# Optimization experiments

Measured on AMD Instinct MI355X. Metric: run time of the kernel, lower is better.

## Reference

```python
import jax, jax.numpy as jnp
import numpy as np

NEG_INF = -100000000.0  # matches masked_fill value in torch source

def setup_inputs() -> dict:
    key = jax.random.key(0)
    ks = jax.random.split(key, 7)
    d_model, d = 1024, 128
    B, S = 4, 2048
    scale = 1.0 / np.sqrt(d_model)
    x = jax.random.normal(ks[0], (B, S, d_model), dtype=jnp.float32)
    Wq = jax.random.normal(ks[1], (d, d_model), dtype=jnp.float32) * scale
    bq = jax.random.normal(ks[2], (d,), dtype=jnp.float32) * 0.02
    Wk = jax.random.normal(ks[3], (d, d_model), dtype=jnp.float32) * scale
    bk = jax.random.normal(ks[4], (d,), dtype=jnp.float32) * 0.02
    Wv = jax.random.normal(ks[5], (d, d_model), dtype=jnp.float32) * scale
    bv = jax.random.normal(ks[6], (d,), dtype=jnp.float32) * 0.02
    return {"x": x, "Wq": Wq, "bq": bq, "Wk": Wk, "bk": bk, "Wv": Wv, "bv": bv}

def reference(x, Wq, bq, Wk, bk, Wv, bv):
    # Q,K,V: [B,S,d] via torch Linear (x @ W.T + b)
    Q = jnp.einsum('bsm,dm->bsd', x, Wq) + bq
    K = jnp.einsum('bsm,dm->bsd', x, Wk) + bk
    V = jnp.einsum('bsm,dm->bsd', x, Wv) + bv
    d = Wk.shape[0]
    scale = 1.0 / jnp.sqrt(jnp.asarray(d, dtype=Q.dtype))
    scores = jnp.einsum('bqd,bkd->bqk', Q, K) * scale  # [B,S,S]
    # Faithful to source: tril then value-based mask (tril==0 -> -1e8).
    tril = jnp.tril(scores)
    masked = jnp.where(tril == 0, NEG_INF, tril)
    attn = jax.nn.softmax(masked, axis=-1)
    context = jnp.einsum('bqk,bkd->bqd', attn, V)
    return context
```

## Files before the change

kernel.cpp:

```cpp
#include <hip/hip_runtime.h>

typedef __attribute__((ext_vector_type(8))) short bf16x8;
typedef __attribute__((ext_vector_type(4))) float f32x4;

__device__ __forceinline__ unsigned short f2bf(float f) {
    unsigned int u = __float_as_uint(f);
    u += 0x7fffu + ((u >> 16) & 1u);
    return (unsigned short)(u >> 16);
}
__device__ __forceinline__ unsigned int pack2bf(float lo, float hi) {
    return (unsigned int)f2bf(lo) | ((unsigned int)f2bf(hi) << 16);
}
__device__ __forceinline__ void async_ld16(void* lds, const void* g) {
    __builtin_amdgcn_global_load_lds(
        (const __attribute__((address_space(1))) unsigned int*)g,
        (__attribute__((address_space(3))) unsigned int*)lds, 16, 0, 0);
}

__global__ __launch_bounds__(256) void conv_w(
    const float* __restrict__ Wq, const float* __restrict__ Wk,
    const float* __restrict__ Wv, unsigned short* __restrict__ Wcat)
{
    size_t o = ((size_t)blockIdx.x * 256 + threadIdx.x) * 8;
    int sel = (int)(o >> 17);
    const float* W = (sel == 0) ? Wq : ((sel == 1) ? Wk : Wv);
    const float* src = W + (o & 131071);
    float4 f0 = ((const float4*)src)[0];
    float4 f1 = ((const float4*)src)[1];
    uint4 u;
    u.x = pack2bf(f0.x, f0.y); u.y = pack2bf(f0.z, f0.w);
    u.z = pack2bf(f1.x, f1.y); u.w = pack2bf(f1.z, f1.w);
    *(uint4*)(Wcat + o) = u;
}

__global__ __launch_bounds__(256) void qkv_gemm(
    const float* __restrict__ x,
    const unsigned short* __restrict__ Wcat,
    const float* __restrict__ bq, const float* __restrict__ bk,
    const float* __restrict__ bv,
    unsigned short* __restrict__ Qg,
    unsigned short* __restrict__ Kg,
    unsigned short* __restrict__ Vtg)
{
    __shared__ unsigned short As[2][32 * 64];
    __shared__ unsigned short Bs[2][128 * 64];

    const int tid  = threadIdx.x;
    const int lane = tid & 63;
    const int w    = tid >> 6;
    const int quad = lane >> 4;
    const int ln   = lane & 15;
    const int lr   = lane >> 3;
    const int csw  = ((lane & 7) ^ lr) * 8;

    const int bid   = blockIdx.x;
    const int nb    = bid >> 8;
    const int mbase = (bid & 255) * 32;
    const unsigned short* Wsel = Wcat + (size_t)nb * 128 * 1024;

    const int arow  = tid >> 3;
    const int achk  = tid & 7;
    const int aslot = achk ^ (arow & 7);
    const float* xsrc = x + (size_t)(mbase + arow) * 1024 + achk * 8;
    unsigned short* adst0 = &As[0][arow * 64 + aslot * 8];
    unsigned short* adst1 = &As[1][arow * 64 + aslot * 8];

    f32x4 acc[2][2];
#pragma unroll
    for (int mt = 0; mt < 2; mt++)
#pragma unroll
        for (int nt = 0; nt < 2; nt++) acc[mt][nt] = (f32x4){0.f, 0.f, 0.f, 0.f};

    auto stageB = [&](int kb, int p) {
        const int kcol = kb * 64 + csw;
#pragma unroll
        for (int j = 0; j < 4; j++) {
            int chunk = w * 4 + j;
            async_ld16(&Bs[p][chunk * 512 + lane * 8],
                       Wsel + (size_t)(chunk * 8 + lr) * 1024 + kcol);
        }
    };
    auto writeA = [&](int p, const float4& f0, const float4& f1) {
        uint4 u;
        u.x = pack2bf(f0.x, f0.y); u.y = pack2bf(f0.z, f0.w);
        u.z = pack2bf(f1.x, f1.y); u.w = pack2bf(f1.z, f1.w);
        *(uint4*)((p == 0) ? adst0 : adst1) = u;
    };

    float4 a0 = ((const float4*)xsrc)[0];
    float4 a1 = ((const float4*)xsrc)[1];
    stageB(0, 0);
    writeA(0, a0, a1);
    __syncthreads();

    for (int kb = 0; kb < 16; kb++) {
        const int p = kb & 1;
        float4 n0, n1;
        if (kb < 15) {
            stageB(kb + 1, p ^ 1);
            const float* xs = xsrc + (kb + 1) * 64;
            n0 = ((const float4*)xs)[0];
            n1 = ((const float4*)xs)[1];
        }
#pragma unroll
        for (int ks = 0; ks < 2; ks++) {
            bf16x8 a[2], b[2];
#pragma unroll
            for (int mt = 0; mt < 2; mt++) {
                int row = mt * 16 + ln;
                a[mt] = *(const bf16x8*)&As[p][row * 64 + ((ks * 4 + quad) ^ (ln & 7)) * 8];
            }
#pragma unroll
            for (int nt = 0; nt < 2; nt++) {
                int row = w * 32 + nt * 16 + ln;
                b[nt] = *(const bf16x8*)&Bs[p][row * 64 + ((ks * 4 + quad) ^ (ln & 7)) * 8];
            }
#pragma unroll
            for (int mt = 0; mt < 2; mt++)
#pragma unroll
                for (int nt = 0; nt < 2; nt++)
                    acc[mt][nt] = __builtin_amdgcn_mfma_f32_16x16x32_bf16(
                        a[mt], b[nt], acc[mt][nt], 0, 0, 0);
        }
        if (kb < 15) writeA(p ^ 1, n0, n1);
        __syncthreads();
    }

    const float scale = (nb == 0) ? 0.08838834764831845f : 1.0f;
    const float* bsel = (nb == 0) ? bq : ((nb == 1) ? bk : bv);
    float bias_v[2];
#pragma unroll
    for (int nt = 0; nt < 2; nt++) bias_v[nt] = bsel[w * 32 + nt * 16 + ln];

    if (nb < 2) {
        unsigned short* dst = (nb == 0) ? Qg : Kg;
#pragma unroll
        for (int mt = 0; mt < 2; mt++)
#pragma unroll
            for (int nt = 0; nt < 2; nt++)
#pragma unroll
                for (int r = 0; r < 4; r++) {
                    int m = mbase + mt * 16 + quad * 4 + r;
                    int d = w * 32 + nt * 16 + ln;
                    dst[(size_t)m * 128 + d] =
                        f2bf((acc[mt][nt][r] + bias_v[nt]) * scale);
                }
    } else {
#pragma unroll
        for (int mt = 0; mt < 2; mt++)
#pragma unroll
            for (int nt = 0; nt < 2; nt++) {
                int dd = w * 32 + nt * 16 + ln;
                int m0 = mbase + mt * 16 + quad * 4;
                int bb = m0 >> 11, s0 = m0 & 2047;
                ushort4 u = { f2bf(acc[mt][nt][0] + bias_v[nt]),
                              f2bf(acc[mt][nt][1] + bias_v[nt]),
                              f2bf(acc[mt][nt][2] + bias_v[nt]),
                              f2bf(acc[mt][nt][3] + bias_v[nt]) };
                *(ushort4*)&Vtg[((size_t)bb * 128 + dd) * 2048 + s0] = u;
            }
    }
}

__global__ __launch_bounds__(256) void flash_attn(
    const unsigned short* __restrict__ Qg,
    const unsigned short* __restrict__ Kg,
    const unsigned short* __restrict__ Vtg,
    unsigned short* __restrict__ Opart,
    float2* __restrict__ ml)
{
    __shared__ unsigned short Ks[2][64 * 128];
    __shared__ unsigned short Vts[2][128 * 64];
    __shared__ unsigned short Pl[64][72];

    const int b = blockIdx.x;
    const int q = blockIdx.y;
    const int c = blockIdx.z;
    const int m4 = q >> 2, r4 = q & 3;
    if (c > m4) return;

    const int pbase = b * 144 + q + 2 * m4 * (m4 - 1) + r4 * m4;
    const int pidx  = pbase + c;
    const int k0 = c * 4;
    const int kend = (c * 4 + 4 < q + 1) ? (c * 4 + 4) : (q + 1);

    const int tid  = threadIdx.x;
    const int lane = tid & 63, w = tid >> 6, quad = lane >> 4, ln = lane & 15;

    bf16x8 qa[4];
    const unsigned short* qrow =
        Qg + ((size_t)b * 2048 + q * 64 + w * 16 + ln) * 128 + quad * 8;
#pragma unroll
    for (int ks = 0; ks < 4; ks++) qa[ks] = *(const bf16x8*)(qrow + ks * 32);

    auto stage = [&](int kt, int p) {
        const unsigned short* ksrc = Kg + ((size_t)b * 2048 + kt * 64) * 128;
        const int krl = lane >> 4;
#pragma unroll
        for (int j = 0; j < 4; j++) {
            int chunk = w * 4 + j;
            int row = chunk * 4 + krl;
            int cd = (lane & 15) ^ (row & 15);
            async_ld16(&Ks[p][chunk * 512 + lane * 8],
                       ksrc + (size_t)row * 128 + cd * 8);
        }
        const unsigned short* vsrc = Vtg + (size_t)b * 128 * 2048 + kt * 64;
        const int vrl = lane >> 3;
#pragma unroll
        for (int j = 0; j < 4; j++) {
            int chunk = w * 4 + j;
            int row = chunk * 8 + vrl;
            int cd = (lane & 7) ^ (row & 7);
            async_ld16(&Vts[p][chunk * 512 + lane * 8],
                       vsrc + (size_t)row * 2048 + cd * 8);
        }
    };

    float m_i[4], l_i[4];
    f32x4 Ofr[8];
#pragma unroll
    for (int r = 0; r < 4; r++) { m_i[r] = -__builtin_inff(); l_i[r] = 0.f; }
#pragma unroll
    for (int dt = 0; dt < 8; dt++) Ofr[dt] = (f32x4){0.f, 0.f, 0.f, 0.f};

    stage(k0, 0);
    __syncthreads();

    int p = 0;
    for (int kt = k0; kt < kend; kt++) {
        if (kt + 1 < kend) stage(kt + 1, p ^ 1);

        f32x4 sfr[4];
#pragma unroll
        for (int ct = 0; ct < 4; ct++) {
            f32x4 s = (f32x4){0.f, 0.f, 0.f, 0.f};
#pragma unroll
            for (int ks = 0; ks < 4; ks++) {
                int row = ct * 16 + ln;
                bf16x8 kf = *(const bf16x8*)&Ks[p][row * 128 + ((ks * 4 + quad) ^ ln) * 8];
                s = __builtin_amdgcn_mfma_f32_16x16x32_bf16(qa[ks], kf, s, 0, 0, 0);
            }
            sfr[ct] = s;
        }

        if (kt == q) {
#pragma unroll
            for (int ct = 0; ct < 4; ct++)
#pragma unroll
                for (int r = 0; r < 4; r++)
                    if (ct * 16 + ln > w * 16 + quad * 4 + r)
                        sfr[ct][r] = -__builtin_inff();
        }

        float mrow[4];
#pragma unroll
        for (int r = 0; r < 4; r++) mrow[r] = -__builtin_inff();
#pragma unroll
        for (int ct = 0; ct < 4; ct++)
#pragma unroll
            for (int r = 0; r < 4; r++) mrow[r] = fmaxf(mrow[r], sfr[ct][r]);
#pragma unroll
        for (int off = 1; off < 16; off <<= 1)
#pragma unroll
            for (int r = 0; r < 4; r++)
                mrow[r] = fmaxf(mrow[r], __shfl_xor(mrow[r], off, 64));

        float alpha[4], rs[4];
#pragma unroll
        for (int r = 0; r < 4; r++) {
            float mn = fmaxf(m_i[r], mrow[r]);
            alpha[r] = __expf(m_i[r] - mn);
            m_i[r]   = mn;
            rs[r]    = 0.f;
        }
#pragma unroll
        for (int ct = 0; ct < 4; ct++)
#pragma unroll
            for (int r = 0; r < 4; r++) {
                float pv = __expf(sfr[ct][r] - m_i[r]);
                rs[r] += pv;
                Pl[w * 16 + quad * 4 + r][ct * 16 + ln] = f2bf(pv);
            }
#pragma unroll
        for (int off = 1; off < 16; off <<= 1)
#pragma unroll
            for (int r = 0; r < 4; r++) rs[r] += __shfl_xor(rs[r], off, 64);
#pragma unroll
        for (int r = 0; r < 4; r++) l_i[r] = l_i[r] * alpha[r] + rs[r];
#pragma unroll
        for (int dt = 0; dt < 8; dt++)
#pragma unroll
            for (int r = 0; r < 4; r++) Ofr[dt][r] *= alpha[r];

#pragma unroll
        for (int kstep = 0; kstep < 2; kstep++) {
            bf16x8 pa = *(const bf16x8*)&Pl[w * 16 + ln][kstep * 32 + quad * 8];
#pragma unroll
            for (int dt = 0; dt < 8; dt++) {
                int row = dt * 16 + ln;
                bf16x8 vf = *(const bf16x8*)&Vts[p][row * 64 + ((kstep * 4 + quad) ^ (ln & 7)) * 8];
                Ofr[dt] = __builtin_amdgcn_mfma_f32_16x16x32_bf16(pa, vf, Ofr[dt], 0, 0, 0);
            }
        }
        __syncthreads();
        p ^= 1;
    }

#pragma unroll
    for (int dt = 0; dt < 8; dt++)
#pragma unroll
        for (int r = 0; r < 4; r++) {
            int row = w * 16 + quad * 4 + r;
            Opart[((size_t)pidx * 64 + row) * 128 + dt * 16 + ln] = f2bf(Ofr[dt][r]);
        }
    if (ln == 0) {
#pragma unroll
        for (int r = 0; r < 4; r++) {
            int row = w * 16 + quad * 4 + r;
            ml[(size_t)pidx * 64 + row] = make_float2(m_i[r], l_i[r]);
        }
    }
}

__global__ __launch_bounds__(256) void combine(
    const unsigned short* __restrict__ Opart,
    const float2* __restrict__ ml,
    float* __restrict__ out)
{
    const int idx  = blockIdx.x >> 1;
    const int half = blockIdx.x & 1;
    const int b = idx >> 5, q = idx & 31;
    const int m4 = q >> 2, r4 = q & 3;
    const int pbase = b * 144 + q + 2 * m4 * (m4 - 1) + r4 * m4;
    const int nc = m4 + 1;

    const int row = threadIdx.x & 63;
    const int grp = half * 64 + (threadIdx.x >> 6) * 16;

    float2 t[8];
#pragma unroll
    for (int c2 = 0; c2 < 8; c2++) {
        int cc = (c2 < nc) ? c2 : (nc - 1);
        t[c2] = ml[(size_t)(pbase + cc) * 64 + row];
    }
    float mc[8], lc[8], wgt[8];
    float mmax = -__builtin_inff();
#pragma unroll
    for (int c2 = 0; c2 < 8; c2++) {
        mc[c2] = (c2 < nc) ? t[c2].x : -__builtin_inff();
        lc[c2] = (c2 < nc) ? t[c2].y : 0.f;
        mmax = fmaxf(mmax, mc[c2]);
    }
    float lsum = 0.f;
#pragma unroll
    for (int c2 = 0; c2 < 8; c2++) {
        wgt[c2] = __expf(mc[c2] - mmax);
        lsum += lc[c2] * wgt[c2];
    }
    const float inv = 1.0f / lsum;

#pragma unroll
    for (int v = 0; v < 2; v++) {
        int col = grp + v * 8;
        float acc[8];
#pragma unroll
        for (int k = 0; k < 8; k++) acc[k] = 0.f;
#pragma unroll
        for (int c2 = 0; c2 < 8; c2++) {
            int cc = (c2 < nc) ? c2 : (nc - 1);
            uint4 u = *(const uint4*)&Opart[((size_t)(pbase + cc) * 64 + row) * 128 + col];
            float wc = wgt[c2];
            acc[0] += wc * __uint_as_float(u.x << 16);
            acc[1] += wc * __uint_as_float(u.x & 0xffff0000u);
            acc[2] += wc * __uint_as_float(u.y << 16);
            acc[3] += wc * __uint_as_float(u.y & 0xffff0000u);
            acc[4] += wc * __uint_as_float(u.z << 16);
            acc[5] += wc * __uint_as_float(u.z & 0xffff0000u);
            acc[6] += wc * __uint_as_float(u.w << 16);
            acc[7] += wc * __uint_as_float(u.w & 0xffff0000u);
        }
        float* o = &out[((size_t)b * 2048 + q * 64 + row) * 128 + col];
        float4 o0 = { acc[0] * inv, acc[1] * inv, acc[2] * inv, acc[3] * inv };
        float4 o1 = { acc[4] * inv, acc[5] * inv, acc[6] * inv, acc[7] * inv };
        ((float4*)o)[0] = o0;
        ((float4*)o)[1] = o1;
    }
}

extern "C" void kernel_launch(void* const* d_in, const int* in_sizes, int n_in,
                              void* d_out, int out_size, void* d_ws, size_t ws_size,
                              hipStream_t stream) {
    const float* x  = (const float*)d_in[0];
    const float* Wq = (const float*)d_in[1];
    const float* bq = (const float*)d_in[2];
    const float* Wk = (const float*)d_in[3];
    const float* bk = (const float*)d_in[4];
    const float* Wv = (const float*)d_in[5];
    const float* bv = (const float*)d_in[6];
    float* out = (float*)d_out;

    char* wsb = (char*)d_ws;
    unsigned short* Opart = (unsigned short*)wsb;
    float2*         ml    = (float2*)(wsb + 9437184);
    unsigned short* Wcat  = (unsigned short*)(wsb + 10485760);
    unsigned short* Qg    = (unsigned short*)(wsb + 11272192);
    unsigned short* Kg    = Qg + (size_t)8192 * 128;
    unsigned short* Vtg   = Qg + (size_t)2 * 8192 * 128;

    conv_w<<<192, 256, 0, stream>>>(Wq, Wk, Wv, Wcat);
    qkv_gemm<<<768, 256, 0, stream>>>(x, Wcat, bq, bk, bv, Qg, Kg, Vtg);
    flash_attn<<<dim3(4, 32, 8), 256, 0, stream>>>(Qg, Kg, Vtg, Opart, ml);
    combine<<<256, 256, 0, stream>>>(Opart, ml, out);
}
```

Baseline: 128.0 us.

## Load K and V fragments directly from global memory instead of LDS staging

The attention kernel no longer double-buffers K and V tiles in shared memory with async global-to-LDS copies. Each wave now reads its MFMA operand fragments for K and V straight from global memory, relying on the caches. This removes the per-tile __syncthreads barriers and roughly 64KB of LDS per block, which can allow more resident blocks. In exchange, all four waves fetch the same K/V data separately, there is no explicit prefetch of the next tile, and the global access patterns are strided rather than coalesced, so load latency may be exposed.

Result: slower. 149.9 us (+17.1%).

```diff
diff --git a/kernel.cpp b/kernel.cpp
--- a/kernel.cpp
+++ b/kernel.cpp
@@ -169,8 +169,6 @@
     unsigned short* __restrict__ Opart,
     float2* __restrict__ ml)
 {
-    __shared__ unsigned short Ks[2][64 * 128];
-    __shared__ unsigned short Vts[2][128 * 64];
     __shared__ unsigned short Pl[64][72];
 
     const int b = blockIdx.x;
@@ -193,28 +191,10 @@
 #pragma unroll
     for (int ks = 0; ks < 4; ks++) qa[ks] = *(const bf16x8*)(qrow + ks * 32);
 
-    auto stage = [&](int kt, int p) {
-        const unsigned short* ksrc = Kg + ((size_t)b * 2048 + kt * 64) * 128;
-        const int krl = lane >> 4;
-#pragma unroll
-        for (int j = 0; j < 4; j++) {
-            int chunk = w * 4 + j;
-            int row = chunk * 4 + krl;
-            int cd = (lane & 15) ^ (row & 15);
-            async_ld16(&Ks[p][chunk * 512 + lane * 8],
-                       ksrc + (size_t)row * 128 + cd * 8);
-        }
-        const unsigned short* vsrc = Vtg + (size_t)b * 128 * 2048 + kt * 64;
-        const int vrl = lane >> 3;
-#pragma unroll
-        for (int j = 0; j < 4; j++) {
-            int chunk = w * 4 + j;
-            int row = chunk * 8 + vrl;
-            int cd = (lane & 7) ^ (row & 7);
-            async_ld16(&Vts[p][chunk * 512 + lane * 8],
-                       vsrc + (size_t)row * 2048 + cd * 8);
-        }
-    };
+    const unsigned short* kbase =
+        Kg + ((size_t)b * 2048 + ln) * 128 + quad * 8;
+    const unsigned short* vbase =
+        Vtg + ((size_t)b * 128 + ln) * 2048 + quad * 8;
 
     float m_i[4], l_i[4];
     f32x4 Ofr[8];
@@ -223,23 +203,19 @@
 #pragma unroll
     for (int dt = 0; dt < 8; dt++) Ofr[dt] = (f32x4){0.f, 0.f, 0.f, 0.f};
 
-    stage(k0, 0);
-    __syncthreads();
-
-    int p = 0;
     for (int kt = k0; kt < kend; kt++) {
-        if (kt + 1 < kend) stage(kt + 1, p ^ 1);
-
+        const unsigned short* kb_t = kbase + (size_t)kt * 64 * 128;
         f32x4 sfr[4];
 #pragma unroll
         for (int ct = 0; ct < 4; ct++) {
+            bf16x8 kf[4];
+#pragma unroll
+            for (int ks = 0; ks < 4; ks++)
+                kf[ks] = *(const bf16x8*)(kb_t + (size_t)ct * 16 * 128 + ks * 32);
             f32x4 s = (f32x4){0.f, 0.f, 0.f, 0.f};
 #pragma unroll
-            for (int ks = 0; ks < 4; ks++) {
-                int row = ct * 16 + ln;
-                bf16x8 kf = *(const bf16x8*)&Ks[p][row * 128 + ((ks * 4 + quad) ^ ln) * 8];
-                s = __builtin_amdgcn_mfma_f32_16x16x32_bf16(qa[ks], kf, s, 0, 0, 0);
-            }
+            for (int ks = 0; ks < 4; ks++)
+                s = __builtin_amdgcn_mfma_f32_16x16x32_bf16(qa[ks], kf[ks], s, 0, 0, 0);
             sfr[ct] = s;
         }
 
@@ -292,18 +268,16 @@
 #pragma unroll
             for (int r = 0; r < 4; r++) Ofr[dt][r] *= alpha[r];
 
+        const unsigned short* vb_t = vbase + kt * 64;
 #pragma unroll
         for (int kstep = 0; kstep < 2; kstep++) {
             bf16x8 pa = *(const bf16x8*)&Pl[w * 16 + ln][kstep * 32 + quad * 8];
 #pragma unroll
             for (int dt = 0; dt < 8; dt++) {
-                int row = dt * 16 + ln;
-                bf16x8 vf = *(const bf16x8*)&Vts[p][row * 64 + ((kstep * 4 + quad) ^ (ln & 7)) * 8];
+                bf16x8 vf = *(const bf16x8*)(vb_t + (size_t)dt * 16 * 2048 + kstep * 32);
                 Ofr[dt] = __builtin_amdgcn_mfma_f32_16x16x32_bf16(pa, vf, Ofr[dt], 0, 0, 0);
             }
         }
-        __syncthreads();
-        p ^= 1;
     }
 
 #pragma unroll
```
